# Optimization experiments

Measured on AMD Instinct MI355X. Metric: run time of the kernel, lower is better.

Reference implementation:

```python
import jax, jax.numpy as jnp
import numpy as np

B_SZ, D, HW, STRIDE, HEADS, DK, DV = 32, 64, 64, 4, 2, 32, 32
N = HW * HW                      # 4096 query tokens
M = (HW // STRIDE) ** 2          # 256 key/value tokens
EPS = 1e-5


def setup_inputs() -> dict:
    key = jax.random.key(0)
    ks = jax.random.split(key, 8)
    w = lambda k, s: jax.random.normal(k, s, dtype=jnp.float32) * 0.02
    return {
        "x": jax.random.normal(ks[0], (B_SZ, D, HW, HW), dtype=jnp.float32),
        "W_dw": jax.random.normal(ks[1], (D, 1, STRIDE, STRIDE), dtype=jnp.float32) * 0.1,
        "b_dw": jnp.zeros((D,), jnp.float32),
        "Wq": w(ks[2], (HEADS * DK, D)), "bq": jnp.zeros((HEADS * DK,), jnp.float32),
        "Wk": w(ks[3], (HEADS * DK, D)), "bk": jnp.zeros((HEADS * DK,), jnp.float32),
        "Wv": w(ks[4], (HEADS * DV, D)), "bv": jnp.zeros((HEADS * DV,), jnp.float32),
        "Wo": w(ks[5], (D, HEADS * DV)), "bo": jnp.zeros((D,), jnp.float32),
        "B": jax.random.normal(ks[6], (1, HEADS, N, M), dtype=jnp.float32),
    }


def reference(x, W_dw, b_dw, Wq, bq, Wk, bk, Wv, bv, Wo, bo, B):
    b, c, h, w = x.shape
    heads = B.shape[1]
    dk = Wq.shape[0] // heads
    dv = Wv.shape[0] // heads
    s = W_dw.shape[-1]

    # LayerNorm over (C, H, W), no affine params
    mu = jnp.mean(x, axis=(1, 2, 3), keepdims=True)
    var = jnp.mean((x - mu) ** 2, axis=(1, 2, 3), keepdims=True)
    xn = (x - mu) * jax.lax.rsqrt(var + EPS)

    # Q from normalized input: (b, N, c)
    xr = jnp.transpose(xn.reshape(b, c, h * w), (0, 2, 1))
    q = (xr @ Wq.T + bq).reshape(b, h * w, heads, dk).transpose(0, 2, 1, 3)

    # K/V from depthwise-conv downsample of the *unnormalized* x (as in source)
    kc = jax.lax.conv_general_dilated(
        x, W_dw, window_strides=(s, s), padding="VALID",
        feature_group_count=c,
        dimension_numbers=("NCHW", "OIHW", "NCHW"),
    ) + b_dw[None, :, None, None]
    kh, kw = kc.shape[2], kc.shape[3]
    kv_in = jnp.transpose(kc.reshape(b, c, kh * kw), (0, 2, 1))  # (b, M, c)
    k = (kv_in @ Wk.T + bk).reshape(b, kh * kw, heads, dk).transpose(0, 2, 1, 3)
    v = (kv_in @ Wv.T + bv).reshape(b, kh * kw, heads, dv).transpose(0, 2, 1, 3)

    # Attention with additive relative bias
    attn = jnp.einsum("bhid,bhjd->bhij", q, k) * (dk ** -0.5) + B
    attn = jax.nn.softmax(attn, axis=-1)
    tmp = jnp.einsum("bhij,bhjd->bhid", attn, v)           # (b, heads, N, dv)
    tmp = tmp.transpose(0, 2, 1, 3).reshape(b, h * w, heads * dv)

    # Output proj; NOTE: source does a raw .view(b, d, h, w) (reshape, not permute)
    out = (tmp @ Wo.T + bo).reshape(b, c, h, w)
    return out + x
```

## Files before the change

kernel.cpp:

```cpp
#include <hip/hip_runtime.h>

typedef float f32x4 __attribute__((ext_vector_type(4)));

#define MFMA8(a, b, c) __builtin_amdgcn_mfma_f32_16x16x32_fp8_fp8((long)(a), (long)(b), (c), 0, 0, 0)

__device__ __forceinline__ unsigned char f2fp8(float v) {
    int pk = __builtin_amdgcn_cvt_pk_fp8_f32(v, v, 0, false);
    return (unsigned char)(pk & 0xff);
}
__device__ __forceinline__ long packrow8(const float* p) {
    f32x4 a = *(const f32x4*)(p);
    f32x4 b = *(const f32x4*)(p + 4);
    int lo = __builtin_amdgcn_cvt_pk_fp8_f32(a.x, a.y, 0, false);
    lo = __builtin_amdgcn_cvt_pk_fp8_f32(a.z, a.w, lo, true);
    int hi = __builtin_amdgcn_cvt_pk_fp8_f32(b.x, b.y, 0, false);
    hi = __builtin_amdgcn_cvt_pk_fp8_f32(b.z, b.w, hi, true);
    return (long)(((unsigned long)(unsigned int)hi << 32) | (unsigned int)lo);
}
__device__ __forceinline__ int pack4(const float* p) {
    int v = __builtin_amdgcn_cvt_pk_fp8_f32(p[0], p[1], 0, false);
    return __builtin_amdgcn_cvt_pk_fp8_f32(p[2], p[3], v, true);
}

__global__ __launch_bounds__(256) void k_ln_part(const float* __restrict__ x,
                                                 float* __restrict__ part) {
    const int chunk = blockIdx.x, b = blockIdx.y, t = threadIdx.x;
    const float4* p = (const float4*)(x + b * 262144 + chunk * 16384);
    float s = 0.f, ss = 0.f;
    #pragma unroll
    for (int r = 0; r < 16; ++r) {
        float4 v = p[r * 256 + t];
        s  += v.x + v.y + v.z + v.w;
        ss += v.x * v.x + v.y * v.y + v.z * v.z + v.w * v.w;
    }
    #pragma unroll
    for (int off = 32; off > 0; off >>= 1) {
        s  += __shfl_down(s, off);
        ss += __shfl_down(ss, off);
    }
    __shared__ float sm[8];
    int wv = t >> 6;
    if ((t & 63) == 0) { sm[wv * 2] = s; sm[wv * 2 + 1] = ss; }
    __syncthreads();
    if (t == 0) {
        float S  = sm[0] + sm[2] + sm[4] + sm[6];
        float SS = sm[1] + sm[3] + sm[5] + sm[7];
        part[(b * 16 + chunk) * 2]     = S;
        part[(b * 16 + chunk) * 2 + 1] = SS;
    }
}

__global__ void k_ln_fin(const float* __restrict__ part, float* __restrict__ stats) {
    int t = threadIdx.x;
    if (t < 32) {
        float S = 0.f, SS = 0.f;
        for (int k = 0; k < 16; ++k) {
            S  += part[(t * 16 + k) * 2];
            SS += part[(t * 16 + k) * 2 + 1];
        }
        const float inv = 1.0f / 262144.0f;
        float mu  = S * inv;
        float var = SS * inv - mu * mu;
        stats[t * 2]     = mu;
        stats[t * 2 + 1] = rsqrtf(var + 1e-5f);
    }
}

__global__ __launch_bounds__(512) void k_kvb2(
    const float* __restrict__ x, const float* __restrict__ Wdw, const float* __restrict__ bdw,
    const float* __restrict__ Wk, const float* __restrict__ bk,
    const float* __restrict__ Wv, const float* __restrict__ bv,
    const float* __restrict__ Wq, const float* __restrict__ Wo,
    unsigned char* __restrict__ Kg, unsigned char* __restrict__ Vg,
    float* __restrict__ part, unsigned char* __restrict__ Wq8, unsigned char* __restrict__ Wo8)
{
    __shared__ __align__(16) unsigned char Y[16 * 72];
    __shared__ float sm[16];
    const int mi = blockIdx.x, b = blockIdx.y;
    const int t = threadIdx.x, w = t >> 6, lane = t & 63;
    const int quad = lane >> 4, l = lane & 15;
    const float* xb = x + b * 262144;

    if ((mi | b) == 0) {
        float f[8];
        #pragma unroll
        for (int g = 0; g < 2; ++g) *(f32x4*)&f[g * 4] = *(const f32x4*)(Wq + t * 8 + g * 4);
        int2 o;
        o.x = pack4(f); o.y = pack4(f + 4);
        *(int2*)(Wq8 + t * 8) = o;
        #pragma unroll
        for (int g = 0; g < 2; ++g) *(f32x4*)&f[g * 4] = *(const f32x4*)(Wo + t * 8 + g * 4);
        o.x = pack4(f); o.y = pack4(f + 4);
        *(int2*)(Wo8 + t * 8) = o;
    }

    const int s2l = lane & 3, mjl = lane >> 2;
    float s = 0.f, ss = 0.f;
    #pragma unroll
    for (int ci = 0; ci < 8; ++ci) {
        int c = w * 8 + ci;
        float wd0 = Wdw[c * 16 + 0 + s2l];
        float wd1 = Wdw[c * 16 + 4 + s2l];
        float wd2 = Wdw[c * 16 + 8 + s2l];
        float wd3 = Wdw[c * 16 + 12 + s2l];
        const float* xr = xb + c * 4096 + mi * 256;
        float v0 = xr[lane], v1 = xr[64 + lane], v2 = xr[128 + lane], v3 = xr[192 + lane];
        s  += v0 + v1 + v2 + v3;
        ss += v0 * v0 + v1 * v1 + v2 * v2 + v3 * v3;
        float acc = v0 * wd0;
        acc = fmaf(v1, wd1, acc);
        acc = fmaf(v2, wd2, acc);
        acc = fmaf(v3, wd3, acc);
        acc += __shfl_xor(acc, 1);
        acc += __shfl_xor(acc, 2);
        if (s2l == 0) Y[mjl * 72 + c] = f2fp8(acc + bdw[c]);
    }
    #pragma unroll
    for (int off = 32; off > 0; off >>= 1) {
        s  += __shfl_down(s, off);
        ss += __shfl_down(ss, off);
    }
    if (lane == 0) { sm[w * 2] = s; sm[w * 2 + 1] = ss; }
    __syncthreads();
    if (t == 0) {
        float S = 0.f, SS = 0.f;
        #pragma unroll
        for (int i = 0; i < 8; ++i) { S += sm[i * 2]; SS += sm[i * 2 + 1]; }
        part[(b * 16 + mi) * 2]     = S;
        part[(b * 16 + mi) * 2 + 1] = SS;
    }

    long ya0 = *(const long*)(Y + l * 72 + quad * 8);
    long ya1 = *(const long*)(Y + l * 72 + 32 + quad * 8);
    if (w < 4) {
        int e4 = w;
        long f0 = packrow8(Wk + (e4 * 16 + l) * 64 + quad * 8);
        long f1 = packrow8(Wk + (e4 * 16 + l) * 64 + 32 + quad * 8);
        float bb = bk[e4 * 16 + l];
        f32x4 c = { bb, bb, bb, bb };
        c = MFMA8(ya0, f0, c);
        c = MFMA8(ya1, f1, c);
        unsigned char* kd = Kg + b * 16384 + (mi * 16 + quad * 4) * 64 + e4 * 16 + l;
        #pragma unroll
        for (int r = 0; r < 4; ++r) kd[r * 64] = f2fp8(c[r]);
    } else {
        int d4 = w - 4;
        long f0 = packrow8(Wv + (d4 * 16 + l) * 64 + quad * 8);
        long f1 = packrow8(Wv + (d4 * 16 + l) * 64 + 32 + quad * 8);
        f32x4 c = { bv[d4 * 16 + quad * 4 + 0], bv[d4 * 16 + quad * 4 + 1],
                    bv[d4 * 16 + quad * 4 + 2], bv[d4 * 16 + quad * 4 + 3] };
        c = MFMA8(f0, ya0, c);
        c = MFMA8(f1, ya1, c);
        unsigned char* vd = Vg + b * 16384 + (d4 * 16 + quad * 4) * 256 + mi * 16 + l;
        #pragma unroll
        for (int r = 0; r < 4; ++r) vd[r * 256] = f2fp8(c[r]);
    }
}

__global__ __launch_bounds__(512, 6) void k_attn3(
    const float* __restrict__ x, const unsigned char* __restrict__ Wq8,
    const float* __restrict__ bq, const unsigned char* __restrict__ Wo8,
    const float* __restrict__ bo, const float* __restrict__ Bb,
    const float* __restrict__ part, const unsigned char* __restrict__ Kg,
    const unsigned char* __restrict__ Vg, float* __restrict__ outp)
{
    __shared__ __align__(16) long smem8[6528];
    unsigned char* S = (unsigned char*)smem8;
    unsigned char* Kf = S;
    unsigned char* Vt = S + 20480;
    unsigned char* XS = S + 37888;
    unsigned char* QF = S + 42496;
    unsigned char* TS = S + 37888;
    const int tile = blockIdx.x, b = blockIdx.y;
    const int t = threadIdx.x, w = t >> 6, lane = t & 63;
    const int quad = lane >> 4, l = lane & 15;
    unsigned char* PS = S + 47104 + w * 640;
    const int n0 = tile * 64;
    const float* xb = x + b * 262144;
    const float SCALE = 0.17677669529663687f;

    float Sp = 0.f, SSp = 0.f;
    #pragma unroll
    for (int k2 = 0; k2 < 16; ++k2) {
        Sp  += part[(b * 16 + k2) * 2];
        SSp += part[(b * 16 + k2) * 2 + 1];
    }
    const float invN = 1.0f / 262144.0f;
    const float mu = Sp * invN;
    const float rstd = rsqrtf(SSp * invN - mu * mu + 1e-5f);

    const unsigned char* Kgb = Kg + b * 16384;
    const unsigned char* Vgb = Vg + b * 16384;
    #pragma unroll
    for (int r = 0; r < 2; ++r) {
        int idx = t + 512 * r;
        int m = idx >> 2, c16 = (idx & 3) * 16;
        *(uint4*)(Kf + m * 80 + c16) = *(const uint4*)(Kgb + m * 64 + c16);
        int d = idx >> 4, e16 = (idx & 15) * 16;
        *(uint4*)(Vt + d * 272 + e16) = *(const uint4*)(Vgb + d * 256 + e16);
    }
    #pragma unroll
    for (int ci = 0; ci < 8; ++ci) {
        int c = w * 8 + ci;
        float v = (xb[c * 4096 + n0 + lane] - mu) * rstd;
        XS[lane * 72 + c] = f2fp8(v);
    }
    const int rtq = w >> 1, ct0 = (w & 1) * 2;
    long wqF[4], woF[4];
    float bqr[2], bor[2];
    #pragma unroll
    for (int i = 0; i < 2; ++i) {
        #pragma unroll
        for (int st = 0; st < 2; ++st) {
            wqF[i * 2 + st] = *(const long*)(Wq8 + ((ct0 + i) * 16 + l) * 64 + st * 32 + quad * 8);
            woF[i * 2 + st] = *(const long*)(Wo8 + ((ct0 + i) * 16 + l) * 64 + st * 32 + quad * 8);
        }
        bqr[i] = bq[(ct0 + i) * 16 + l];
        bor[i] = bo[(ct0 + i) * 16 + l];
    }
    __syncthreads();

    {
        long xa0 = *(const long*)(XS + (rtq * 16 + l) * 72 + quad * 8);
        long xa1 = *(const long*)(XS + (rtq * 16 + l) * 72 + 32 + quad * 8);
        #pragma unroll
        for (int i = 0; i < 2; ++i) {
            f32x4 c = { bqr[i], bqr[i], bqr[i], bqr[i] };
            c = MFMA8(xa0, wqF[i * 2 + 0], c);
            c = MFMA8(xa1, wqF[i * 2 + 1], c);
            unsigned char* qd = QF + (rtq * 16 + quad * 4) * 72 + (ct0 + i) * 16 + l;
            #pragma unroll
            for (int r = 0; r < 4; ++r) qd[r * 72] = f2fp8(c[r]);
        }
    }
    __syncthreads();

    const int h = w & 1, nq = w >> 1;
    long qa = *(const long*)(QF + (nq * 16 + l) * 72 + h * 32 + quad * 8);
    f32x4 O0 = { 0, 0, 0, 0 }, O1 = { 0, 0, 0, 0 };
    float Lp[4] = { 0, 0, 0, 0 };
    const float* Bbase = Bb + h * 1048576 + (n0 + nq * 16 + quad * 4) * 256;

    float Bv[2][4];
    #pragma unroll
    for (int sub = 0; sub < 2; ++sub)
        #pragma unroll
        for (int r = 0; r < 4; ++r)
            Bv[sub][r] = Bbase[r * 256 + sub * 16 + l];

    #pragma unroll 2
    for (int mc = 0; mc < 8; ++mc) {
        float Bn[2][4];
        if (mc < 7) {
            #pragma unroll
            for (int sub = 0; sub < 2; ++sub)
                #pragma unroll
                for (int r = 0; r < 4; ++r)
                    Bn[sub][r] = Bbase[r * 256 + (mc * 2 + 2 + sub) * 16 + l];
        }
        long kb0 = *(const long*)(Kf + ((mc * 2 + 0) * 16 + l) * 80 + h * 32 + quad * 8);
        long kb1 = *(const long*)(Kf + ((mc * 2 + 1) * 16 + l) * 80 + h * 32 + quad * 8);
        #pragma unroll
        for (int sub = 0; sub < 2; ++sub) {
            f32x4 sc = { 0, 0, 0, 0 };
            sc = MFMA8(qa, sub ? kb1 : kb0, sc);
            unsigned char* pw = PS + (quad * 4) * 40 + sub * 16 + l;
            #pragma unroll
            for (int r = 0; r < 4; ++r) {
                float p = __expf(fmaf(sc[r], SCALE, Bv[sub][r]));
                Lp[r] += p;
                pw[r * 40] = f2fp8(p);
            }
        }
        long pa  = *(const long*)(PS + l * 40 + quad * 8);
        long vb0 = *(const long*)(Vt + (h * 32 + l) * 272 + mc * 32 + quad * 8);
        long vb1 = *(const long*)(Vt + (h * 32 + 16 + l) * 272 + mc * 32 + quad * 8);
        O0 = MFMA8(pa, vb0, O0);
        O1 = MFMA8(pa, vb1, O1);
        #pragma unroll
        for (int sub = 0; sub < 2; ++sub)
            #pragma unroll
            for (int r = 0; r < 4; ++r)
                Bv[sub][r] = Bn[sub][r];
    }
    #pragma unroll
    for (int r = 0; r < 4; ++r) {
        #pragma unroll
        for (int d = 1; d < 16; d <<= 1) Lp[r] += __shfl_xor(Lp[r], d);
    }
    {
        unsigned char* td = TS + (nq * 16 + quad * 4) * 72 + h * 32 + l;
        #pragma unroll
        for (int r = 0; r < 4; ++r) {
            float inv = 1.0f / Lp[r];
            td[r * 72]      = f2fp8(O0[r] * inv);
            td[r * 72 + 16] = f2fp8(O1[r] * inv);
        }
    }
    __syncthreads();

    {
        long ta0 = *(const long*)(TS + (rtq * 16 + l) * 72 + quad * 8);
        long ta1 = *(const long*)(TS + (rtq * 16 + l) * 72 + 32 + quad * 8);
        float* ob = outp + b * 262144 + tile * 4096;
        const float* xr2 = xb + tile * 4096;
        #pragma unroll
        for (int i = 0; i < 2; ++i) {
            f32x4 c = { bor[i], bor[i], bor[i], bor[i] };
            c = MFMA8(ta0, woF[i * 2 + 0], c);
            c = MFMA8(ta1, woF[i * 2 + 1], c);
            #pragma unroll
            for (int r = 0; r < 4; ++r) {
                int off = (rtq * 16 + quad * 4 + r) * 64 + (ct0 + i) * 16 + l;
                ob[off] = c[r] + xr2[off];
            }
        }
    }
}

__global__ __launch_bounds__(512) void k_fused(
    const float* __restrict__ x, const float* __restrict__ Wdw, const float* __restrict__ bdw,
    const float* __restrict__ Wq, const float* __restrict__ bq,
    const float* __restrict__ Wk, const float* __restrict__ bk,
    const float* __restrict__ Wv, const float* __restrict__ bv,
    const float* __restrict__ Wo, const float* __restrict__ bo,
    const float* __restrict__ Bb, const float* __restrict__ stats,
    float* __restrict__ outp)
{
    __shared__ long smem8[6784];
    unsigned char* S = (unsigned char*)smem8;
    unsigned char* Kf = S;
    unsigned char* Vt = S + 18432;
    unsigned char* Y  = S + 35328;
    unsigned char* XS = S + 35328;
    unsigned char* QF = S + 35328 + 4608;
    unsigned char* TS = S + 35328 + 14336;

    const int tg = blockIdx.x, b = blockIdx.y;
    const int t = threadIdx.x, w = t >> 6, lane = t & 63;
    const int quad = lane >> 4, l = lane & 15;
    unsigned char* PS = S + 35328 + 9216 + w * 640;

    const float mu = stats[2 * b], rstd = stats[2 * b + 1];
    const float* xb = x + b * 262144;
    const float SCALE = 0.17677669529663687f;

    long wkF[8], wvF[8];
    #pragma unroll
    for (int e4 = 0; e4 < 4; ++e4)
        #pragma unroll
        for (int st = 0; st < 2; ++st) {
            wkF[e4 * 2 + st] = packrow8(Wk + (e4 * 16 + l) * 64 + st * 32 + quad * 8);
            wvF[e4 * 2 + st] = packrow8(Wv + (e4 * 16 + l) * 64 + st * 32 + quad * 8);
        }
    const int rtq = w >> 1, ct0 = (w & 1) * 2;
    long wqF[4], woF[4];
    #pragma unroll
    for (int i = 0; i < 2; ++i)
        #pragma unroll
        for (int st = 0; st < 2; ++st) {
            wqF[i * 2 + st] = packrow8(Wq + ((ct0 + i) * 16 + l) * 64 + st * 32 + quad * 8);
            woF[i * 2 + st] = packrow8(Wo + ((ct0 + i) * 16 + l) * 64 + st * 32 + quad * 8);
        }
    float bkr[4], bvr[4][4], bqr[2], bor[2];
    #pragma unroll
    for (int e4 = 0; e4 < 4; ++e4) bkr[e4] = bk[e4 * 16 + l];
    #pragma unroll
    for (int d4 = 0; d4 < 4; ++d4)
        #pragma unroll
        for (int r = 0; r < 4; ++r) bvr[d4][r] = bv[d4 * 16 + quad * 4 + r];
    #pragma unroll
    for (int i = 0; i < 2; ++i) { bqr[i] = bq[(ct0 + i) * 16 + l]; bor[i] = bo[(ct0 + i) * 16 + l]; }

    {
        const int s2l = lane & 3, mjl = lane >> 2;
        for (int ci = 0; ci < 8; ++ci) {
            int c = w * 8 + ci;
            float wd0 = Wdw[c * 16 + 0 + s2l];
            float wd1 = Wdw[c * 16 + 4 + s2l];
            float wd2 = Wdw[c * 16 + 8 + s2l];
            float wd3 = Wdw[c * 16 + 12 + s2l];
            float bdc = bdw[c];
            #pragma unroll 4
            for (int mi = 0; mi < 16; ++mi) {
                const float* xr = xb + c * 4096 + mi * 256;
                float acc = xr[lane] * wd0;
                acc = fmaf(xr[64 + lane],  wd1, acc);
                acc = fmaf(xr[128 + lane], wd2, acc);
                acc = fmaf(xr[192 + lane], wd3, acc);
                acc += __shfl_xor(acc, 1);
                acc += __shfl_xor(acc, 2);
                if (s2l == 0) Y[(mi * 16 + mjl) * 72 + c] = f2fp8(acc + bdc);
            }
        }
    }
    __syncthreads();

    #pragma unroll
    for (int i = 0; i < 2; ++i) {
        int rt = w * 2 + i;
        long ya0 = *(const long*)(Y + (rt * 16 + l) * 72 + quad * 8);
        long ya1 = *(const long*)(Y + (rt * 16 + l) * 72 + 32 + quad * 8);
        #pragma unroll
        for (int e4 = 0; e4 < 4; ++e4) {
            f32x4 c = { bkr[e4], bkr[e4], bkr[e4], bkr[e4] };
            c = MFMA8(ya0, wkF[e4 * 2 + 0], c);
            c = MFMA8(ya1, wkF[e4 * 2 + 1], c);
            unsigned char* kd = Kf + (rt * 16 + quad * 4) * 72 + e4 * 16 + l;
            #pragma unroll
            for (int r = 0; r < 4; ++r) kd[r * 72] = f2fp8(c[r]);
        }
        #pragma unroll
        for (int d4 = 0; d4 < 4; ++d4) {
            f32x4 c = { bvr[d4][0], bvr[d4][1], bvr[d4][2], bvr[d4][3] };
            c = MFMA8(wvF[d4 * 2 + 0], ya0, c);
            c = MFMA8(wvF[d4 * 2 + 1], ya1, c);
            unsigned char* vd = Vt + (d4 * 16 + quad * 4) * 264 + rt * 16 + l;
            #pragma unroll
            for (int r = 0; r < 4; ++r) vd[r * 264] = f2fp8(c[r]);
        }
    }
    __syncthreads();

    const int h = w & 1, nq = w >> 1;

    for (int tile = 0; tile < 8; ++tile) {
        const int tidx = tg * 8 + tile, n0 = tidx * 64;

        for (int ci = 0; ci < 8; ++ci) {
            int c = w * 8 + ci;
            float v = (xb[c * 4096 + n0 + lane] - mu) * rstd;
            XS[lane * 72 + c] = f2fp8(v);
        }
        __syncthreads();

        {
            long xa0 = *(const long*)(XS + (rtq * 16 + l) * 72 + quad * 8);
            long xa1 = *(const long*)(XS + (rtq * 16 + l) * 72 + 32 + quad * 8);
            #pragma unroll
            for (int i = 0; i < 2; ++i) {
                f32x4 c = { bqr[i], bqr[i], bqr[i], bqr[i] };
                c = MFMA8(xa0, wqF[i * 2 + 0], c);
                c = MFMA8(xa1, wqF[i * 2 + 1], c);
                unsigned char* qd = QF + (rtq * 16 + quad * 4) * 72 + (ct0 + i) * 16 + l;
                #pragma unroll
                for (int r = 0; r < 4; ++r) qd[r * 72] = f2fp8(c[r]);
            }
        }
        __syncthreads();

        long qa = *(const long*)(QF + (nq * 16 + l) * 72 + h * 32 + quad * 8);
        f32x4 O0 = { 0, 0, 0, 0 }, O1 = { 0, 0, 0, 0 };
        float Lp[4] = { 0, 0, 0, 0 };
        const float* Bbase = Bb + h * 1048576 + (n0 + nq * 16 + quad * 4) * 256;

        #pragma unroll 2
        for (int mc = 0; mc < 8; ++mc) {
            #pragma unroll
            for (int sub = 0; sub < 2; ++sub) {
                int mt = mc * 2 + sub;
                long kb = *(const long*)(Kf + (mt * 16 + l) * 72 + h * 32 + quad * 8);
                f32x4 sc = { 0, 0, 0, 0 };
                sc = MFMA8(qa, kb, sc);
                unsigned char* pw = PS + (quad * 4) * 40 + sub * 16 + l;
                #pragma unroll
                for (int r = 0; r < 4; ++r) {
                    float p = __expf(fmaf(sc[r], SCALE, Bbase[r * 256 + mt * 16 + l]));
                    Lp[r] += p;
                    pw[r * 40] = f2fp8(p);
                }
            }
            long pa  = *(const long*)(PS + l * 40 + quad * 8);
            long vb0 = *(const long*)(Vt + (h * 32 + l) * 264 + mc * 32 + quad * 8);
            long vb1 = *(const long*)(Vt + (h * 32 + 16 + l) * 264 + mc * 32 + quad * 8);
            O0 = MFMA8(pa, vb0, O0);
            O1 = MFMA8(pa, vb1, O1);
        }
        #pragma unroll
        for (int r = 0; r < 4; ++r) {
            #pragma unroll
            for (int d = 1; d < 16; d <<= 1) Lp[r] += __shfl_xor(Lp[r], d);
        }
        {
            unsigned char* td = TS + (nq * 16 + quad * 4) * 72 + h * 32 + l;
            #pragma unroll
            for (int r = 0; r < 4; ++r) {
                float inv = 1.0f / Lp[r];
                td[r * 72]      = f2fp8(O0[r] * inv);
                td[r * 72 + 16] = f2fp8(O1[r] * inv);
            }
        }
        __syncthreads();

        {
            long ta0 = *(const long*)(TS + (rtq * 16 + l) * 72 + quad * 8);
            long ta1 = *(const long*)(TS + (rtq * 16 + l) * 72 + 32 + quad * 8);
            float* ob = outp + b * 262144 + tidx * 4096;
            const float* xr2 = xb + tidx * 4096;
            #pragma unroll
            for (int i = 0; i < 2; ++i) {
                f32x4 c = { bor[i], bor[i], bor[i], bor[i] };
                c = MFMA8(ta0, woF[i * 2 + 0], c);
                c = MFMA8(ta1, woF[i * 2 + 1], c);
                #pragma unroll
                for (int r = 0; r < 4; ++r) {
                    int off = (rtq * 16 + quad * 4 + r) * 64 + (ct0 + i) * 16 + l;
                    ob[off] = c[r] + xr2[off];
                }
            }
        }
        __syncthreads();
    }
}

extern "C" void kernel_launch(void* const* d_in, const int* in_sizes, int n_in,
                              void* d_out, int out_size, void* d_ws, size_t ws_size,
                              hipStream_t stream) {
    (void)in_sizes; (void)n_in; (void)out_size;
    const float* x   = (const float*)d_in[0];
    const float* Wdw = (const float*)d_in[1];
    const float* bdw = (const float*)d_in[2];
    const float* Wq  = (const float*)d_in[3];
    const float* bq  = (const float*)d_in[4];
    const float* Wk  = (const float*)d_in[5];
    const float* bk  = (const float*)d_in[6];
    const float* Wv  = (const float*)d_in[7];
    const float* bv  = (const float*)d_in[8];
    const float* Wo  = (const float*)d_in[9];
    const float* bo  = (const float*)d_in[10];
    const float* Bb  = (const float*)d_in[11];
    float* outp = (float*)d_out;

    float* ws    = (float*)d_ws;
    float* part  = ws;
    float* stats = ws + 1024;
    unsigned char* Wq8 = (unsigned char*)d_ws + 8192;
    unsigned char* Wo8 = (unsigned char*)d_ws + 12288;
    unsigned char* Kg  = (unsigned char*)d_ws + 16384;
    unsigned char* Vg  = Kg + 524288;

    if (ws_size >= (size_t)(16384 + 2 * 524288)) {
        k_kvb2<<<dim3(16, 32), 512, 0, stream>>>(x, Wdw, bdw, Wk, bk, Wv, bv, Wq, Wo,
                                                 Kg, Vg, part, Wq8, Wo8);
        k_attn3<<<dim3(64, 32), 512, 0, stream>>>(x, Wq8, bq, Wo8, bo, Bb, part, Kg, Vg, outp);
    } else {
        k_ln_part<<<dim3(16, 32), 256, 0, stream>>>(x, part);
        k_ln_fin<<<1, 64, 0, stream>>>(part, stats);
        k_fused<<<dim3(8, 32), 512, 0, stream>>>(x, Wdw, bdw, Wq, bq, Wk, bk, Wv, bv,
                                                 Wo, bo, Bb, stats, outp);
    }
}
```

Baseline: 147.4 us.

## Pre-transpose bias into log2-scaled layout and use exp2 in attention

The first kernel now also transposes the relative bias B into an (h, m, n) layout and pre-multiplies it by log2(e), writing it to workspace. The attention kernel then reads the bias with 16-byte vector loads along n instead of scalar strided loads, and computes softmax weights with exp2 using a scale folded with log2(e). This targets the uncoalesced bias reads in the attention loop. In exchange it adds an 8 MB workspace write and read on every call, and requires a larger workspace or the code falls back to the old path.

Result: slower. 159.1 us (+7.9%).

```diff
diff --git a/kernel.cpp b/kernel.cpp
--- a/kernel.cpp
+++ b/kernel.cpp
@@ -3,6 +3,12 @@
 typedef float f32x4 __attribute__((ext_vector_type(4)));
 
 #define MFMA8(a, b, c) __builtin_amdgcn_mfma_f32_16x16x32_fp8_fp8((long)(a), (long)(b), (c), 0, 0, 0)
+
+#if __has_builtin(__builtin_amdgcn_exp2f)
+#define EXP2F __builtin_amdgcn_exp2f
+#else
+#define EXP2F exp2f
+#endif
 
 __device__ __forceinline__ unsigned char f2fp8(float v) {
     int pk = __builtin_amdgcn_cvt_pk_fp8_f32(v, v, 0, false);
@@ -71,15 +77,25 @@
     const float* __restrict__ Wk, const float* __restrict__ bk,
     const float* __restrict__ Wv, const float* __restrict__ bv,
     const float* __restrict__ Wq, const float* __restrict__ Wo,
+    const float* __restrict__ Bb, float* __restrict__ Bt,
     unsigned char* __restrict__ Kg, unsigned char* __restrict__ Vg,
     float* __restrict__ part, unsigned char* __restrict__ Wq8, unsigned char* __restrict__ Wo8)
 {
     __shared__ __align__(16) unsigned char Y[16 * 72];
     __shared__ float sm[16];
+    __shared__ float TT[64][65];
     const int mi = blockIdx.x, b = blockIdx.y;
     const int t = threadIdx.x, w = t >> 6, lane = t & 63;
     const int quad = lane >> 4, l = lane & 15;
     const float* xb = x + b * 262144;
+
+    const int tid = b * 16 + mi;
+    const int hB = tid >> 8, rest = tid & 255;
+    const int ntile = rest >> 2, mtile = rest & 3;
+    const int rr = t >> 3, c8 = (t & 7) * 8;
+    const float* Bsrc = Bb + hB * 1048576 + (ntile * 64 + rr) * 256 + mtile * 64 + c8;
+    f32x4 a0 = *(const f32x4*)(Bsrc);
+    f32x4 a1 = *(const f32x4*)(Bsrc + 4);
 
     if ((mi | b) == 0) {
         float f[8];
@@ -155,12 +171,27 @@
         #pragma unroll
         for (int r = 0; r < 4; ++r) vd[r * 256] = f2fp8(c[r]);
     }
+
+    #pragma unroll
+    for (int k = 0; k < 4; ++k) TT[rr][c8 + k] = a0[k];
+    #pragma unroll
+    for (int k = 0; k < 4; ++k) TT[rr][c8 + 4 + k] = a1[k];
+    __syncthreads();
+    {
+        const float LOG2E = 1.4426950408889634f;
+        float o[8];
+        #pragma unroll
+        for (int k = 0; k < 8; ++k) o[k] = TT[c8 + k][rr] * LOG2E;
+        float* Btd = Bt + hB * 1048576 + (mtile * 64 + rr) * 4096 + ntile * 64 + c8;
+        *(f32x4*)(Btd)     = *(f32x4*)&o[0];
+        *(f32x4*)(Btd + 4) = *(f32x4*)&o[4];
+    }
 }
 
 __global__ __launch_bounds__(512, 6) void k_attn3(
     const float* __restrict__ x, const unsigned char* __restrict__ Wq8,
     const float* __restrict__ bq, const unsigned char* __restrict__ Wo8,
-    const float* __restrict__ bo, const float* __restrict__ Bb,
+    const float* __restrict__ bo, const float* __restrict__ Bt,
     const float* __restrict__ part, const unsigned char* __restrict__ Kg,
     const unsigned char* __restrict__ Vg, float* __restrict__ outp)
 {
@@ -177,7 +208,7 @@
     unsigned char* PS = S + 47104 + w * 640;
     const int n0 = tile * 64;
     const float* xb = x + b * 262144;
-    const float SCALE = 0.17677669529663687f;
+    const float SCALE2 = 0.2550348626f;
 
     float Sp = 0.f, SSp = 0.f;
     #pragma unroll
@@ -239,24 +270,17 @@
     long qa = *(const long*)(QF + (nq * 16 + l) * 72 + h * 32 + quad * 8);
     f32x4 O0 = { 0, 0, 0, 0 }, O1 = { 0, 0, 0, 0 };
     float Lp[4] = { 0, 0, 0, 0 };
-    const float* Bbase = Bb + h * 1048576 + (n0 + nq * 16 + quad * 4) * 256;
-
-    float Bv[2][4];
-    #pragma unroll
-    for (int sub = 0; sub < 2; ++sub)
-        #pragma unroll
-        for (int r = 0; r < 4; ++r)
-            Bv[sub][r] = Bbase[r * 256 + sub * 16 + l];
+    const float* Btb = Bt + h * 1048576 + l * 4096 + n0 + nq * 16 + quad * 4;
+
+    f32x4 Bv0 = *(const f32x4*)(Btb);
+    f32x4 Bv1 = *(const f32x4*)(Btb + 65536);
 
     #pragma unroll 2
     for (int mc = 0; mc < 8; ++mc) {
-        float Bn[2][4];
+        f32x4 Bn0, Bn1;
         if (mc < 7) {
-            #pragma unroll
-            for (int sub = 0; sub < 2; ++sub)
-                #pragma unroll
-                for (int r = 0; r < 4; ++r)
-                    Bn[sub][r] = Bbase[r * 256 + (mc * 2 + 2 + sub) * 16 + l];
+            Bn0 = *(const f32x4*)(Btb + (mc * 2 + 2) * 65536);
+            Bn1 = *(const f32x4*)(Btb + (mc * 2 + 3) * 65536);
         }
         long kb0 = *(const long*)(Kf + ((mc * 2 + 0) * 16 + l) * 80 + h * 32 + quad * 8);
         long kb1 = *(const long*)(Kf + ((mc * 2 + 1) * 16 + l) * 80 + h * 32 + quad * 8);
@@ -267,7 +291,7 @@
             unsigned char* pw = PS + (quad * 4) * 40 + sub * 16 + l;
             #pragma unroll
             for (int r = 0; r < 4; ++r) {
-                float p = __expf(fmaf(sc[r], SCALE, Bv[sub][r]));
+                float p = EXP2F(fmaf(sc[r], SCALE2, sub ? Bv1[r] : Bv0[r]));
                 Lp[r] += p;
                 pw[r * 40] = f2fp8(p);
             }
@@ -277,11 +301,8 @@
         long vb1 = *(const long*)(Vt + (h * 32 + 16 + l) * 272 + mc * 32 + quad * 8);
         O0 = MFMA8(pa, vb0, O0);
         O1 = MFMA8(pa, vb1, O1);
-        #pragma unroll
-        for (int sub = 0; sub < 2; ++sub)
-            #pragma unroll
-            for (int r = 0; r < 4; ++r)
-                Bv[sub][r] = Bn[sub][r];
+        Bv0 = Bn0;
+        Bv1 = Bn1;
     }
     #pragma unroll
     for (int r = 0; r < 4; ++r) {
@@ -538,11 +559,12 @@
     unsigned char* Wo8 = (unsigned char*)d_ws + 12288;
     unsigned char* Kg  = (unsigned char*)d_ws + 16384;
     unsigned char* Vg  = Kg + 524288;
-
-    if (ws_size >= (size_t)(16384 + 2 * 524288)) {
+    float* Bt = (float*)((unsigned char*)d_ws + 2097152);
+
+    if (ws_size >= (size_t)(2097152 + 8388608)) {
         k_kvb2<<<dim3(16, 32), 512, 0, stream>>>(x, Wdw, bdw, Wk, bk, Wv, bv, Wq, Wo,
-                                                 Kg, Vg, part, Wq8, Wo8);
-        k_attn3<<<dim3(64, 32), 512, 0, stream>>>(x, Wq8, bq, Wo8, bo, Bb, part, Kg, Vg, outp);
+                                                 Bb, Bt, Kg, Vg, part, Wq8, Wo8);
+        k_attn3<<<dim3(64, 32), 512, 0, stream>>>(x, Wq8, bq, Wo8, bo, Bt, part, Kg, Vg, outp);
     } else {
         k_ln_part<<<dim3(16, 32), 256, 0, stream>>>(x, part);
         k_ln_fin<<<1, 64, 0, stream>>>(part, stats);
```

## Shrink attention LDS footprint with XOR-swizzled K and direct x fragment loads

Applied to the files above, without the earlier changes.

K is now written to global memory in an XOR-swizzled layout, so it can be copied into shared memory unpadded (64-byte rows instead of 80) while still avoiding bank conflicts. The normalized-x staging buffer is removed: each lane loads its Q-projection A-fragment straight from global and packs it to fp8 in registers. The P scratch now reuses the Q/T region, guarded by extra barriers. Together these cut shared memory per block from about 51KB to 38KB and raise the launch-bounds occupancy hint from 6 to 8, at the cost of strided uncoalesced x loads and two more __syncthreads.

Result: faster. 143.8 us (-2.5%).

```diff
diff --git a/kernel.cpp b/kernel.cpp
--- a/kernel.cpp
+++ b/kernel.cpp
@@ -20,6 +20,13 @@
 __device__ __forceinline__ int pack4(const float* p) {
     int v = __builtin_amdgcn_cvt_pk_fp8_f32(p[0], p[1], 0, false);
     return __builtin_amdgcn_cvt_pk_fp8_f32(p[2], p[3], v, true);
+}
+__device__ __forceinline__ long pack8v(const float* p) {
+    int lo = __builtin_amdgcn_cvt_pk_fp8_f32(p[0], p[1], 0, false);
+    lo = __builtin_amdgcn_cvt_pk_fp8_f32(p[2], p[3], lo, true);
+    int hi = __builtin_amdgcn_cvt_pk_fp8_f32(p[4], p[5], 0, false);
+    hi = __builtin_amdgcn_cvt_pk_fp8_f32(p[6], p[7], hi, true);
+    return (long)(((unsigned long)(unsigned int)hi << 32) | (unsigned int)lo);
 }
 
 __global__ __launch_bounds__(256) void k_ln_part(const float* __restrict__ x,
@@ -140,9 +147,13 @@
         f32x4 c = { bb, bb, bb, bb };
         c = MFMA8(ya0, f0, c);
         c = MFMA8(ya1, f1, c);
-        unsigned char* kd = Kg + b * 16384 + (mi * 16 + quad * 4) * 64 + e4 * 16 + l;
-        #pragma unroll
-        for (int r = 0; r < 4; ++r) kd[r * 64] = f2fp8(c[r]);
+        unsigned char* kdB = Kg + b * 16384;
+        int colk = e4 * 16 + l;
+        #pragma unroll
+        for (int r = 0; r < 4; ++r) {
+            int row = mi * 16 + quad * 4 + r;
+            kdB[row * 64 + (colk ^ ((row & 7) << 3))] = f2fp8(c[r]);
+        }
     } else {
         int d4 = w - 4;
         long f0 = packrow8(Wv + (d4 * 16 + l) * 64 + quad * 8);
@@ -157,24 +168,23 @@
     }
 }
 
-__global__ __launch_bounds__(512, 6) void k_attn3(
+__global__ __launch_bounds__(512, 8) void k_attn5(
     const float* __restrict__ x, const unsigned char* __restrict__ Wq8,
     const float* __restrict__ bq, const unsigned char* __restrict__ Wo8,
     const float* __restrict__ bo, const float* __restrict__ Bb,
     const float* __restrict__ part, const unsigned char* __restrict__ Kg,
     const unsigned char* __restrict__ Vg, float* __restrict__ outp)
 {
-    __shared__ __align__(16) long smem8[6528];
+    __shared__ __align__(16) long smem8[4864];
     unsigned char* S = (unsigned char*)smem8;
     unsigned char* Kf = S;
-    unsigned char* Vt = S + 20480;
-    unsigned char* XS = S + 37888;
-    unsigned char* QF = S + 42496;
-    unsigned char* TS = S + 37888;
+    unsigned char* Vt = S + 16384;
+    unsigned char* QF = S + 33792;
+    unsigned char* TS = S + 33792;
     const int tile = blockIdx.x, b = blockIdx.y;
     const int t = threadIdx.x, w = t >> 6, lane = t & 63;
     const int quad = lane >> 4, l = lane & 15;
-    unsigned char* PS = S + 47104 + w * 640;
+    unsigned char* PS = S + 33792 + w * 640;
     const int n0 = tile * 64;
     const float* xb = x + b * 262144;
     const float SCALE = 0.17677669529663687f;
@@ -191,20 +201,15 @@
 
     const unsigned char* Kgb = Kg + b * 16384;
     const unsigned char* Vgb = Vg + b * 16384;
+    *(uint4*)(Kf + t * 16)        = *(const uint4*)(Kgb + t * 16);
+    *(uint4*)(Kf + 8192 + t * 16) = *(const uint4*)(Kgb + 8192 + t * 16);
     #pragma unroll
     for (int r = 0; r < 2; ++r) {
         int idx = t + 512 * r;
-        int m = idx >> 2, c16 = (idx & 3) * 16;
-        *(uint4*)(Kf + m * 80 + c16) = *(const uint4*)(Kgb + m * 64 + c16);
         int d = idx >> 4, e16 = (idx & 15) * 16;
         *(uint4*)(Vt + d * 272 + e16) = *(const uint4*)(Vgb + d * 256 + e16);
     }
-    #pragma unroll
-    for (int ci = 0; ci < 8; ++ci) {
-        int c = w * 8 + ci;
-        float v = (xb[c * 4096 + n0 + lane] - mu) * rstd;
-        XS[lane * 72 + c] = f2fp8(v);
-    }
+
     const int rtq = w >> 1, ct0 = (w & 1) * 2;
     long wqF[4], woF[4];
     float bqr[2], bor[2];
@@ -218,28 +223,40 @@
         bqr[i] = bq[(ct0 + i) * 16 + l];
         bor[i] = bo[(ct0 + i) * 16 + l];
     }
-    __syncthreads();
-
+
+    long xa0, xa1;
     {
-        long xa0 = *(const long*)(XS + (rtq * 16 + l) * 72 + quad * 8);
-        long xa1 = *(const long*)(XS + (rtq * 16 + l) * 72 + 32 + quad * 8);
-        #pragma unroll
-        for (int i = 0; i < 2; ++i) {
-            f32x4 c = { bqr[i], bqr[i], bqr[i], bqr[i] };
-            c = MFMA8(xa0, wqF[i * 2 + 0], c);
-            c = MFMA8(xa1, wqF[i * 2 + 1], c);
-            unsigned char* qd = QF + (rtq * 16 + quad * 4) * 72 + (ct0 + i) * 16 + l;
-            #pragma unroll
-            for (int r = 0; r < 4; ++r) qd[r * 72] = f2fp8(c[r]);
-        }
+        const float* xq = xb + n0 + rtq * 16 + l;
+        float xn[8];
+        #pragma unroll
+        for (int j = 0; j < 8; ++j)
+            xn[j] = (xq[(quad * 8 + j) * 4096] - mu) * rstd;
+        xa0 = pack8v(xn);
+        #pragma unroll
+        for (int j = 0; j < 8; ++j)
+            xn[j] = (xq[(32 + quad * 8 + j) * 4096] - mu) * rstd;
+        xa1 = pack8v(xn);
+    }
+    #pragma unroll
+    for (int i = 0; i < 2; ++i) {
+        f32x4 c = { bqr[i], bqr[i], bqr[i], bqr[i] };
+        c = MFMA8(xa0, wqF[i * 2 + 0], c);
+        c = MFMA8(xa1, wqF[i * 2 + 1], c);
+        unsigned char* qd = QF + (rtq * 16 + quad * 4) * 72 + (ct0 + i) * 16 + l;
+        #pragma unroll
+        for (int r = 0; r < 4; ++r) qd[r * 72] = f2fp8(c[r]);
     }
     __syncthreads();
 
     const int h = w & 1, nq = w >> 1;
     long qa = *(const long*)(QF + (nq * 16 + l) * 72 + h * 32 + quad * 8);
+    __syncthreads();
+
     f32x4 O0 = { 0, 0, 0, 0 }, O1 = { 0, 0, 0, 0 };
     float Lp[4] = { 0, 0, 0, 0 };
     const float* Bbase = Bb + h * 1048576 + (n0 + nq * 16 + quad * 4) * 256;
+
+    const unsigned char* Kfl = Kf + l * 64 + ((h * 32 + quad * 8) ^ ((l & 7) << 3));
 
     float Bv[2][4];
     #pragma unroll
@@ -258,8 +275,8 @@
                 for (int r = 0; r < 4; ++r)
                     Bn[sub][r] = Bbase[r * 256 + (mc * 2 + 2 + sub) * 16 + l];
         }
-        long kb0 = *(const long*)(Kf + ((mc * 2 + 0) * 16 + l) * 80 + h * 32 + quad * 8);
-        long kb1 = *(const long*)(Kf + ((mc * 2 + 1) * 16 + l) * 80 + h * 32 + quad * 8);
+        long kb0 = *(const long*)(Kfl + (mc * 2 + 0) * 1024);
+        long kb1 = *(const long*)(Kfl + (mc * 2 + 1) * 1024);
         #pragma unroll
         for (int sub = 0; sub < 2; ++sub) {
             f32x4 sc = { 0, 0, 0, 0 };
@@ -288,6 +305,7 @@
         #pragma unroll
         for (int d = 1; d < 16; d <<= 1) Lp[r] += __shfl_xor(Lp[r], d);
     }
+    __syncthreads();
     {
         unsigned char* td = TS + (nq * 16 + quad * 4) * 72 + h * 32 + l;
         #pragma unroll
@@ -542,7 +560,7 @@
     if (ws_size >= (size_t)(16384 + 2 * 524288)) {
         k_kvb2<<<dim3(16, 32), 512, 0, stream>>>(x, Wdw, bdw, Wk, bk, Wv, bv, Wq, Wo,
                                                  Kg, Vg, part, Wq8, Wo8);
-        k_attn3<<<dim3(64, 32), 512, 0, stream>>>(x, Wq8, bq, Wo8, bo, Bb, part, Kg, Vg, outp);
+        k_attn5<<<dim3(64, 32), 512, 0, stream>>>(x, Wq8, bq, Wo8, bo, Bb, part, Kg, Vg, outp);
     } else {
         k_ln_part<<<dim3(16, 32), 256, 0, stream>>>(x, part);
         k_ln_fin<<<1, 64, 0, stream>>>(part, stats);
```
